# Kernel optimization log

Hardware: AMD Instinct MI355X
Metric: run time of the kernel (lower is better)

The kernel has to match this reference:

```python
import jax, jax.numpy as jnp
import numpy as np

N_NODES = 50000
N_EDGES = 800000
D = 128          # node_dim == hidden_dim (heads=1, concat -> hidden_dim)
N_LAYERS = 3
NUM_GRAPHS = 512


def setup_inputs() -> dict:
    key = jax.random.key(0)
    ks = jax.random.split(key, 12)
    x = jax.random.normal(ks[0], (N_NODES, D), dtype=jnp.float32)
    edge_index = jax.random.randint(ks[1], (2, N_EDGES), 0, N_NODES, dtype=jnp.int64)
    batch = jnp.sort(jax.random.randint(ks[2], (N_NODES,), 0, NUM_GRAPHS, dtype=jnp.int64))
    s = 1.0 / np.sqrt(D)
    # stacked per-layer params (all layers are D->D since node_dim==hidden_dim)
    Wq = jax.random.normal(ks[3], (N_LAYERS, D, D), dtype=jnp.float32) * s
    Wk = jax.random.normal(ks[4], (N_LAYERS, D, D), dtype=jnp.float32) * s
    Wv = jax.random.normal(ks[5], (N_LAYERS, D, D), dtype=jnp.float32) * s
    Ws = jax.random.normal(ks[6], (N_LAYERS, D, D), dtype=jnp.float32) * s  # lin_skip (root weight)
    bq = jnp.zeros((N_LAYERS, D), dtype=jnp.float32)
    bk = jnp.zeros((N_LAYERS, D), dtype=jnp.float32)
    bv = jnp.zeros((N_LAYERS, D), dtype=jnp.float32)
    bs = jnp.zeros((N_LAYERS, D), dtype=jnp.float32)
    return dict(x=x, edge_index=edge_index, batch=batch,
                Wq=Wq, bq=bq, Wk=Wk, bk=bk, Wv=Wv, bv=bv, Ws=Ws, bs=bs)


def _transformer_conv(x, src, dst, Wq, bq, Wk, bk, Wv, bv, Ws, bs):
    # PyG TransformerConv, heads=1, concat=True, root_weight=True, no edge_attr
    q = x @ Wq.T + bq                     # [N, D]
    k = x @ Wk.T + bk                     # [N, D]
    v = x @ Wv.T + bv                     # [N, D]
    scale = 1.0 / jnp.sqrt(jnp.asarray(D, x.dtype))
    alpha = jnp.sum(q[dst] * k[src], axis=-1) * scale           # [E]
    # scatter-softmax over edges sharing the same destination node
    amax = jax.ops.segment_max(alpha, dst, num_segments=N_NODES)  # [N]
    ex = jnp.exp(alpha - amax[dst])                               # [E]
    denom = jax.ops.segment_sum(ex, dst, num_segments=N_NODES)    # [N]
    w = ex / denom[dst]                                           # [E]
    out = jax.ops.segment_sum(w[:, None] * v[src], dst, num_segments=N_NODES)  # [N, D]
    return out + (x @ Ws.T + bs)          # skip connection (lin_skip)


def reference(x, edge_index, batch, Wq, bq, Wk, bk, Wv, bv, Ws, bs):
    src, dst = edge_index[0], edge_index[1]
    for l in range(N_LAYERS):
        x = jax.nn.relu(_transformer_conv(x, src, dst,
                                          Wq[l], bq[l], Wk[l], bk[l],
                                          Wv[l], bv[l], Ws[l], bs[l]))
    # global_mean_pool
    sums = jax.ops.segment_sum(x, batch, num_segments=NUM_GRAPHS)          # [G, D]
    counts = jax.ops.segment_sum(jnp.ones((x.shape[0],), x.dtype), batch,
                                 num_segments=NUM_GRAPHS)                  # [G]
    return sums / jnp.maximum(counts, 1.0)[:, None]
```

## Files before the change

kernel.cpp:

```cpp
#include <hip/hip_runtime.h>
#include <hip/hip_fp8.h>

#define N_NODES 50000
#define N_EDGES 800000
#define DIM 128
#define NLAYERS 3
#define NGRAPH 512
#define SCAN_NB ((N_NODES + 255) / 256)
#define NBUCK   ((N_NODES + 255) / 256)
#define P1_CHUNK 2048
#define P1_EPT   8
#define P1_NB    ((N_EDGES + P1_CHUNK - 1) / P1_CHUNK)

typedef __attribute__((ext_vector_type(8)))  __bf16 bf16x8;
typedef __attribute__((ext_vector_type(16))) float  f32x16;
typedef __attribute__((ext_vector_type(2)))  float  f32x2;

union U8 { uint2 u; unsigned char b[8]; };

__device__ inline void cvt8_pk(U8 x, f32x2* f) {
#if defined(__has_builtin) && __has_builtin(__builtin_amdgcn_cvt_pk_f32_fp8)
    f[0] = __builtin_amdgcn_cvt_pk_f32_fp8(x.u.x, false);
    f[1] = __builtin_amdgcn_cvt_pk_f32_fp8(x.u.x, true);
    f[2] = __builtin_amdgcn_cvt_pk_f32_fp8(x.u.y, false);
    f[3] = __builtin_amdgcn_cvt_pk_f32_fp8(x.u.y, true);
#else
#pragma unroll
    for (int j = 0; j < 4; ++j) {
        __hip_fp8_e4m3 a; a.__x = x.b[2 * j];
        __hip_fp8_e4m3 c; c.__x = x.b[2 * j + 1];
        f32x2 r; r[0] = (float)a; r[1] = (float)c;
        f[j] = r;
    }
#endif
}

__device__ inline uint4 pack16_fp8(const float* v) {
    uint4 r;
    unsigned int* pr = (unsigned int*)&r;
#if defined(__has_builtin) && __has_builtin(__builtin_amdgcn_cvt_pk_fp8_f32)
#pragma unroll
    for (int w = 0; w < 4; ++w) {
        int o = 0;
        o = __builtin_amdgcn_cvt_pk_fp8_f32(v[4 * w + 0], v[4 * w + 1], o, false);
        o = __builtin_amdgcn_cvt_pk_fp8_f32(v[4 * w + 2], v[4 * w + 3], o, true);
        pr[w] = (unsigned int)o;
    }
#else
#pragma unroll
    for (int w = 0; w < 4; ++w) {
        unsigned int o = 0;
#pragma unroll
        for (int j = 0; j < 4; ++j) {
            __hip_fp8_e4m3 t8(v[4 * w + j]);
            o |= ((unsigned int)t8.__x) << (8 * j);
        }
        pr[w] = o;
    }
#endif
    return r;
}

__global__ __launch_bounds__(256) void k_cast(const float* __restrict__ in,
                                              __bf16* __restrict__ out, int n) {
    int i = blockIdx.x * blockDim.x + threadIdx.x;
    int base = i * 8;
    if (base >= n) return;
    float4 a = *(const float4*)(in + base);
    float4 b = *(const float4*)(in + base + 4);
    bf16x8 o;
    o[0] = (__bf16)a.x; o[1] = (__bf16)a.y; o[2] = (__bf16)a.z; o[3] = (__bf16)a.w;
    o[4] = (__bf16)b.x; o[5] = (__bf16)b.y; o[6] = (__bf16)b.z; o[7] = (__bf16)b.w;
    *(bf16x8*)(out + base) = o;
}

__global__ __launch_bounds__(256) void k_castW(
    const float* __restrict__ i0, const float* __restrict__ i1,
    const float* __restrict__ i2, const float* __restrict__ i3,
    __bf16* __restrict__ o0, __bf16* __restrict__ o1,
    __bf16* __restrict__ o2, __bf16* __restrict__ o3) {
    int sel = blockIdx.y;
    const float* in = (sel == 0) ? i0 : (sel == 1) ? i1 : (sel == 2) ? i2 : i3;
    __bf16* out     = (sel == 0) ? o0 : (sel == 1) ? o1 : (sel == 2) ? o2 : o3;
    int i = blockIdx.x * 256 + threadIdx.x;
    if (i >= NLAYERS * 2048) return;
    int layer = i >> 11;
    int w = i & 2047;
    int ct = w >> 9, kt = (w >> 6) & 7, lane = w & 63;
    int row = ct * 32 + (lane & 31);
    int col = kt * 16 + (lane >> 5) * 8;
    const float* srcp = in + (size_t)layer * DIM * DIM + row * DIM + col;
    float4 a = *(const float4*)srcp;
    float4 b = *(const float4*)(srcp + 4);
    bf16x8 o;
    o[0] = (__bf16)a.x; o[1] = (__bf16)a.y; o[2] = (__bf16)a.z; o[3] = (__bf16)a.w;
    o[4] = (__bf16)b.x; o[5] = (__bf16)b.y; o[6] = (__bf16)b.z; o[7] = (__bf16)b.w;
    *(bf16x8*)(out + (size_t)i * 8) = o;
}

__global__ __launch_bounds__(256) void k_degree(const int* __restrict__ dst,
                                                int* __restrict__ cnt) {
    int i = blockIdx.x * blockDim.x + threadIdx.x;
    if (i < N_EDGES) atomicAdd(&cnt[dst[i]], 1);
}

__global__ __launch_bounds__(256) void k_scan1(const int* __restrict__ cnt,
                                               int* __restrict__ off,
                                               int* __restrict__ bsum) {
    __shared__ int s[256];
    int b = blockIdx.x, t = threadIdx.x;
    int i = b * 256 + t;
    int v = (i < N_NODES) ? cnt[i] : 0;
    s[t] = v; __syncthreads();
#pragma unroll
    for (int d = 1; d < 256; d <<= 1) {
        int nv = (t >= d) ? s[t - d] : 0;
        __syncthreads();
        s[t] += nv;
        __syncthreads();
    }
    if (i < N_NODES) off[i] = s[t] - v;
    if (t == 255) bsum[b] = s[255];
}

__global__ __launch_bounds__(256) void k_scan2(const int* __restrict__ bsum,
                                               int* __restrict__ boff,
                                               int* __restrict__ offN) {
    __shared__ int s[256];
    int t = threadIdx.x;
    int v = (t < SCAN_NB) ? bsum[t] : 0;
    s[t] = v; __syncthreads();
#pragma unroll
    for (int d = 1; d < 256; d <<= 1) {
        int nv = (t >= d) ? s[t - d] : 0;
        __syncthreads();
        s[t] += nv;
        __syncthreads();
    }
    boff[t] = s[t] - v;
    if (t == 255) *offN = s[255];
}

__global__ __launch_bounds__(256) void k_scan3(int* __restrict__ off,
                                               const int* __restrict__ boff) {
    int b = blockIdx.x, t = threadIdx.x;
    int i = b * 256 + t;
    if (i < N_NODES) off[i] += boff[b];
}

__global__ __launch_bounds__(256) void k_ginit(const int* __restrict__ off,
                                               int* __restrict__ gcursor) {
    int t = threadIdx.x;
    if (t < NBUCK) gcursor[t] = off[t * 256];
}

__global__ __launch_bounds__(256) void k_bucket(const int* __restrict__ src,
                                                const int* __restrict__ dst,
                                                int* __restrict__ gcursor,
                                                unsigned long long* __restrict__ pairs) {
    __shared__ int lcount[256];
    __shared__ int lstart[256];
    __shared__ int lresv[256];
    __shared__ unsigned long long stage[P1_CHUNK];
    int t = threadIdx.x;
    int base = blockIdx.x * P1_CHUNK;
    int cnt = N_EDGES - base; if (cnt > P1_CHUNK) cnt = P1_CHUNK;

    lcount[t] = 0;
    __syncthreads();

    int my_s[P1_EPT], my_d[P1_EPT], my_b[P1_EPT];
#pragma unroll
    for (int j = 0; j < P1_EPT; ++j) {
        int idx = t + j * 256;
        if (idx < cnt) {
            my_s[j] = src[base + idx];
            my_d[j] = dst[base + idx];
            my_b[j] = my_d[j] >> 8;
            atomicAdd(&lcount[my_b[j]], 1);
        } else my_b[j] = -1;
    }
    __syncthreads();

    int v = lcount[t];
    lstart[t] = v;
    __syncthreads();
#pragma unroll
    for (int d = 1; d < 256; d <<= 1) {
        int nv = (t >= d) ? lstart[t - d] : 0;
        __syncthreads();
        lstart[t] += nv;
        __syncthreads();
    }
    int excl = lstart[t] - v;
    __syncthreads();
    lstart[t] = excl;
    lresv[t] = (t < NBUCK && v > 0) ? atomicAdd(&gcursor[t], v) : 0;
    lcount[t] = 0;
    __syncthreads();

#pragma unroll
    for (int j = 0; j < P1_EPT; ++j) {
        if (my_b[j] >= 0) {
            int lpos = lstart[my_b[j]] + atomicAdd(&lcount[my_b[j]], 1);
            stage[lpos] = ((unsigned long long)(unsigned)my_d[j] << 32) | (unsigned)my_s[j];
        }
    }
    __syncthreads();

    for (int sl = t; sl < cnt; sl += 256) {
        unsigned long long pr = stage[sl];
        int d_ = (int)(pr >> 32);
        int b_ = d_ >> 8;
        int g = lresv[b_] + (sl - lstart[b_]);
        pairs[g] = pr;
    }
}

__global__ __launch_bounds__(256) void k_csr(const unsigned long long* __restrict__ pairs,
                                             const int* __restrict__ off,
                                             int* __restrict__ src_s) {
    __shared__ int cur[256];
    int b = blockIdx.x, t = threadIdx.x;
    int nb0 = b * 256;
    int nb1 = nb0 + 256; if (nb1 > N_NODES) nb1 = N_NODES;
    int e0 = off[nb0], e1 = off[nb1];
    cur[t] = 0;
    __syncthreads();
    for (int e = e0 + t; e < e1; e += 256) {
        unsigned long long pr = pairs[e];
        int d_ = (int)(pr >> 32);
        int s_ = (int)(pr & 0xffffffffu);
        int pos = off[d_] + atomicAdd(&cur[d_ & 255], 1);
        src_s[pos] = s_;
    }
}

__global__ __launch_bounds__(256) void k_gemm_fused(
    const __bf16* __restrict__ Xb,
    const __bf16* __restrict__ Wq, const __bf16* __restrict__ Wk,
    const __bf16* __restrict__ Wv, const __bf16* __restrict__ Wsk,
    const float* __restrict__ Bq, const float* __restrict__ Bk,
    const float* __restrict__ Bv, const float* __restrict__ Bs,
    __bf16* __restrict__ Oq, unsigned char* __restrict__ Okv,
    __bf16* __restrict__ Osk) {
    __shared__ uint4 At[32][16];
    __shared__ float lt[4][32][33];
    int t = threadIdx.x;
    int wsel = t >> 6, l = t & 63;
    int lo5 = l & 31, hi = l >> 5;
    int row0 = blockIdx.x * 32;

    const __bf16* W = (wsel == 0) ? Wq : (wsel == 1) ? Wk : (wsel == 2) ? Wv : Wsk;
    const float*  B = (wsel == 0) ? Bq : (wsel == 1) ? Bk : (wsel == 2) ? Bv : Bs;

    {
        int r = t >> 3;
        int u0 = (t & 7) * 2;
        int grow = row0 + r;
        uint4 a0 = {}, a1 = {};
        if (grow < N_NODES) {
            const uint4* gp = (const uint4*)(Xb + (size_t)grow * DIM);
            a0 = gp[u0]; a1 = gp[u0 + 1];
        }
        At[r][u0 ^ (r & 15)]       = a0;
        At[r][(u0 + 1) ^ (r & 15)] = a1;
    }
    __syncthreads();

    bf16x8 a[8];
#pragma unroll
    for (int kt = 0; kt < 8; ++kt)
        a[kt] = *(const bf16x8*)&At[lo5][(kt * 2 + hi) ^ (lo5 & 15)];

    int rr = l >> 1, h = l & 1;
    int grow = row0 + rr;
    bool rok = (grow < N_NODES);

#pragma unroll
    for (int ct = 0; ct < 4; ++ct) {
        int col0 = ct * 32;
        const bf16x8* bp = (const bf16x8*)W + (size_t)(ct * 8) * 64 + l;
        f32x16 acc0 = {}, acc1 = {};
#pragma unroll
        for (int kt = 0; kt < 4; ++kt) {
            acc0 = __builtin_amdgcn_mfma_f32_32x32x16_bf16(a[kt],     bp[(size_t)kt * 64],       acc0, 0, 0, 0);
            acc1 = __builtin_amdgcn_mfma_f32_32x32x16_bf16(a[kt + 4], bp[(size_t)(kt + 4) * 64], acc1, 0, 0, 0);
        }
        f32x16 acc = acc0 + acc1;

        float bias = B[col0 + lo5];
#pragma unroll
        for (int r = 0; r < 16; ++r) {
            int rl = (r & 3) + 8 * (r >> 2) + 4 * hi;
            lt[wsel][rl][lo5] = acc[r] + bias;
        }
        __syncthreads();

        float vals[16];
#pragma unroll
        for (int j = 0; j < 16; ++j) vals[j] = lt[wsel][rr][h * 16 + j];

        if (rok) {
            int gcol = col0 + h * 16;
            if (wsel == 0 || wsel == 3) {
                __bf16* O = (wsel == 0) ? Oq : Osk;
                bf16x8 o0, o1;
#pragma unroll
                for (int j = 0; j < 8; ++j) { o0[j] = (__bf16)vals[j]; o1[j] = (__bf16)vals[8 + j]; }
                bf16x8* orow = (bf16x8*)(O + (size_t)grow * DIM + gcol);
                orow[0] = o0; orow[1] = o1;
            } else {
                int coff = (wsel == 2) ? 128 : 0;
                uint4 pk = pack16_fp8(vals);
                *(uint4*)(Okv + (size_t)grow * 256 + coff + gcol) = pk;
            }
        }
        __syncthreads();
    }
}

__global__ __launch_bounds__(256) void k_edge_fused(const __bf16* __restrict__ q,
                                                    const unsigned char* __restrict__ kv,
                                                    const __bf16* __restrict__ skip,
                                                    const int* __restrict__ src_s,
                                                    const int* __restrict__ off,
                                                    float* __restrict__ xout,
                                                    __bf16* __restrict__ xb,
                                                    int wf32) {
    int t = threadIdx.x;
    int wave = t >> 6, l = t & 63;
    int n = blockIdx.x * 4 + wave;
    if (n >= N_NODES) return;
    int g = l >> 4, gl = l & 15;
    int start = off[n], end = off[n + 1];

    const float S = 0.08838834764831845f;
    f32x2 qf[4];
    {
        bf16x8 qv = *(const bf16x8*)(q + (size_t)n * DIM + gl * 8);
#pragma unroll
        for (int j = 0; j < 4; ++j) {
            f32x2 r;
            r[0] = (float)qv[2 * j] * S;
            r[1] = (float)qv[2 * j + 1] * S;
            qf[j] = r;
        }
    }

    float denom = 0.f;
    f32x2 facc[4] = {};

    for (int e = start + g; e < end; e += 8) {
        int s0 = src_s[e];
        bool h1 = (e + 4 < end);
        int s1 = h1 ? src_s[e + 4] : s0;
        const unsigned char* r0 = kv + (size_t)s0 * 256 + gl * 8;
        const unsigned char* r1 = kv + (size_t)s1 * 256 + gl * 8;
        U8 k0u, k1u, v0u, v1u;
        k0u.u = *(const uint2*)(r0);
        k1u.u = *(const uint2*)(r1);
        v0u.u = *(const uint2*)(r0 + 128);
        v1u.u = *(const uint2*)(r1 + 128);

        f32x2 k0f[4], k1f[4];
        cvt8_pk(k0u, k0f);
        cvt8_pk(k1u, k1f);
        f32x2 d0 = qf[0] * k0f[0];
        f32x2 d1 = qf[0] * k1f[0];
        d0 += qf[1] * k0f[1];  d1 += qf[1] * k1f[1];
        d0 += qf[2] * k0f[2];  d1 += qf[2] * k1f[2];
        d0 += qf[3] * k0f[3];  d1 += qf[3] * k1f[3];
        float p0 = d0[0] + d0[1];
        float p1 = d1[0] + d1[1];
        p0 += __shfl_xor(p0, 8, 16);  p1 += __shfl_xor(p1, 8, 16);
        p0 += __shfl_xor(p0, 4, 16);  p1 += __shfl_xor(p1, 4, 16);
        p0 += __shfl_xor(p0, 2, 16);  p1 += __shfl_xor(p1, 2, 16);
        p0 += __shfl_xor(p0, 1, 16);  p1 += __shfl_xor(p1, 1, 16);
        p0 = fminf(p0, 80.f);
        p1 = h1 ? fminf(p1, 80.f) : -INFINITY;

        float w0 = __expf(p0);
        float w1 = __expf(p1);
        denom += w0 + w1;

        f32x2 v0f[4], v1f[4];
        cvt8_pk(v0u, v0f);
        cvt8_pk(v1u, v1f);
        f32x2 w02; w02[0] = w0; w02[1] = w0;
        f32x2 w12; w12[0] = w1; w12[1] = w1;
#pragma unroll
        for (int j = 0; j < 4; ++j)
            facc[j] += w02 * v0f[j] + w12 * v1f[j];
    }

#pragma unroll
    for (int dlt = 16; dlt <= 32; dlt <<= 1) {
        denom += __shfl_xor(denom, dlt, 64);
#pragma unroll
        for (int j = 0; j < 4; ++j) {
            f32x2 o;
            o[0] = __shfl_xor(facc[j][0], dlt, 64);
            o[1] = __shfl_xor(facc[j][1], dlt, 64);
            facc[j] += o;
        }
    }
    float inv = (denom > 0.f) ? 1.f / denom : 0.f;

    if (g == 0) {
        bf16x8 sk = *(const bf16x8*)(skip + (size_t)n * DIM + gl * 8);
        float o[8];
        bf16x8 ob;
#pragma unroll
        for (int j = 0; j < 8; ++j) {
            float f = facc[j >> 1][j & 1];
            float val = fmaxf((float)sk[j] + f * inv, 0.f);
            o[j] = val; ob[j] = (__bf16)val;
        }
        if (wf32) {
            float* xrow = xout + (size_t)n * DIM + gl * 8;
            *(float4*)(xrow)     = make_float4(o[0], o[1], o[2], o[3]);
            *(float4*)(xrow + 4) = make_float4(o[4], o[5], o[6], o[7]);
        }
        *(bf16x8*)(xb + (size_t)n * DIM + gl * 8) = ob;
    }
}

__global__ __launch_bounds__(256) void k_pool(const float* __restrict__ x,
                                              const int* __restrict__ batch,
                                              float* __restrict__ out) {
    __shared__ float sacc[4][DIM];
    int g = blockIdx.x;
    int t = threadIdx.x;
    int w = t >> 6, l = t & 63;
    int lo = 0, hi = N_NODES;
    while (lo < hi) { int mid = (lo + hi) >> 1; if (batch[mid] < g) lo = mid + 1; else hi = mid; }
    int s0 = lo;
    hi = N_NODES;
    while (lo < hi) { int mid = (lo + hi) >> 1; if (batch[mid] < g + 1) lo = mid + 1; else hi = mid; }
    int s1 = lo;
    float a0 = 0.f, a1 = 0.f;
    for (int n = s0 + w; n < s1; n += 4) {
        float2 xr = *(const float2*)(x + (size_t)n * DIM + l * 2);
        a0 += xr.x; a1 += xr.y;
    }
    sacc[w][l * 2] = a0; sacc[w][l * 2 + 1] = a1;
    __syncthreads();
    if (t < DIM) {
        float s = sacc[0][t] + sacc[1][t] + sacc[2][t] + sacc[3][t];
        int cnt = s1 - s0;
        out[(size_t)g * DIM + t] = s / (float)((cnt > 0) ? cnt : 1);
    }
}

extern "C" void kernel_launch(void* const* d_in, const int* in_sizes, int n_in,
                              void* d_out, int out_size, void* d_ws, size_t ws_size,
                              hipStream_t stream) {
    const float* x0   = (const float*)d_in[0];
    const int*  eidx  = (const int*)d_in[1];
    const int*  batch = (const int*)d_in[2];
    const float* Wq = (const float*)d_in[3];
    const float* bq = (const float*)d_in[4];
    const float* Wk = (const float*)d_in[5];
    const float* bk = (const float*)d_in[6];
    const float* Wv = (const float*)d_in[7];
    const float* bv = (const float*)d_in[8];
    const float* Ws = (const float*)d_in[9];
    const float* bs = (const float*)d_in[10];
    float* out = (float*)d_out;

    const int* src = eidx;
    const int* dst = eidx + N_EDGES;

    char* ws = (char*)d_ws;
    size_t p = 0;
    auto alloc = [&](size_t bytes) -> void* {
        void* r = ws + p;
        p = (p + bytes + 255) & ~(size_t)255;
        return r;
    };
    int*    off    = (int*)alloc((N_NODES + 1) * sizeof(int));
    int*    cnt    = (int*)alloc(N_NODES * sizeof(int));
    int*    bsum   = (int*)alloc(256 * sizeof(int));
    int*    boff   = (int*)alloc(256 * sizeof(int));
    int*    gcur   = (int*)alloc(256 * sizeof(int));
    int*    src_s  = (int*)alloc(N_EDGES * sizeof(int));
    unsigned long long* prs = (unsigned long long*)alloc((size_t)N_EDGES * 8);
    __bf16* Xb     = (__bf16*)alloc((size_t)N_NODES * DIM * sizeof(__bf16));
    __bf16* qb     = (__bf16*)alloc((size_t)N_NODES * DIM * sizeof(__bf16));
    unsigned char* kvb = (unsigned char*)alloc((size_t)N_NODES * 256);
    __bf16* skb    = (__bf16*)alloc((size_t)N_NODES * DIM * sizeof(__bf16));
    float*  s1     = (float*)alloc((size_t)N_NODES * DIM * sizeof(float));
    __bf16* Wqb    = (__bf16*)alloc((size_t)NLAYERS * DIM * DIM * sizeof(__bf16));
    __bf16* Wkb    = (__bf16*)alloc((size_t)NLAYERS * DIM * DIM * sizeof(__bf16));
    __bf16* Wvb    = (__bf16*)alloc((size_t)NLAYERS * DIM * DIM * sizeof(__bf16));
    __bf16* Wsb    = (__bf16*)alloc((size_t)NLAYERS * DIM * DIM * sizeof(__bf16));

    {
        int nx = N_NODES * DIM;
        k_cast<<<(nx / 8 + 255) / 256, 256, 0, stream>>>(x0, Xb, nx);
        dim3 gw((NLAYERS * 2048 + 255) / 256, 4);
        k_castW<<<gw, 256, 0, stream>>>(Wq, Wk, Wv, Ws, Wqb, Wkb, Wvb, Wsb);
    }

    hipMemsetAsync(cnt, 0, N_NODES * sizeof(int), stream);
    k_degree<<<(N_EDGES + 255) / 256, 256, 0, stream>>>(dst, cnt);
    k_scan1<<<SCAN_NB, 256, 0, stream>>>(cnt, off, bsum);
    k_scan2<<<1, 256, 0, stream>>>(bsum, boff, off + N_NODES);
    k_scan3<<<SCAN_NB, 256, 0, stream>>>(off, boff);
    k_ginit<<<1, 256, 0, stream>>>(off, gcur);
    k_bucket<<<P1_NB, 256, 0, stream>>>(src, dst, gcur, prs);
    k_csr<<<NBUCK, 256, 0, stream>>>(prs, off, src_s);

    for (int l = 0; l < NLAYERS; ++l) {
        const __bf16* wq = Wqb + (size_t)l * DIM * DIM;
        const __bf16* wk = Wkb + (size_t)l * DIM * DIM;
        const __bf16* wv = Wvb + (size_t)l * DIM * DIM;
        const __bf16* wsk = Wsb + (size_t)l * DIM * DIM;
        const float* biq = bq + (size_t)l * DIM;
        const float* bik = bk + (size_t)l * DIM;
        const float* biv = bv + (size_t)l * DIM;
        const float* bis = bs + (size_t)l * DIM;

        k_gemm_fused<<<(N_NODES + 31) / 32, 256, 0, stream>>>(Xb, wq, wk, wv, wsk,
                                                              biq, bik, biv, bis,
                                                              qb, kvb, skb);
        int wf32 = (l == NLAYERS - 1) ? 1 : 0;
        k_edge_fused<<<(N_NODES + 3) / 4, 256, 0, stream>>>(qb, kvb, skb, src_s, off,
                                                            s1, Xb, wf32);
    }

    k_pool<<<NGRAPH, 256, 0, stream>>>(s1, batch, out);
}
```

Baseline: 278.2 us.

## Interleave K/V fp8 rows and unroll edge gather to four edges per iteration

The projection kernel now writes K and V fp8 values interleaved in 16-byte units (8 K bytes then 8 V bytes per 8 columns), so the edge kernel fetches each lane's K and V slices with one 16-byte load instead of two separate 8-byte loads. The edge loop also processes four edges per group per iteration instead of two, giving more independent gathers in flight to hide memory latency. The costs are higher register pressure and more masked work on the tail for nodes with low degree.

```diff
diff --git a/kernel.cpp b/kernel.cpp
--- a/kernel.cpp
+++ b/kernel.cpp
@@ -35,12 +35,12 @@
 #endif
 }
 
-__device__ inline uint4 pack16_fp8(const float* v) {
-    uint4 r;
+__device__ inline uint2 pack8_fp8(const float* v) {
+    uint2 r;
     unsigned int* pr = (unsigned int*)&r;
 #if defined(__has_builtin) && __has_builtin(__builtin_amdgcn_cvt_pk_fp8_f32)
 #pragma unroll
-    for (int w = 0; w < 4; ++w) {
+    for (int w = 0; w < 2; ++w) {
         int o = 0;
         o = __builtin_amdgcn_cvt_pk_fp8_f32(v[4 * w + 0], v[4 * w + 1], o, false);
         o = __builtin_amdgcn_cvt_pk_fp8_f32(v[4 * w + 2], v[4 * w + 3], o, true);
@@ -48,7 +48,7 @@
     }
 #else
 #pragma unroll
-    for (int w = 0; w < 4; ++w) {
+    for (int w = 0; w < 2; ++w) {
         unsigned int o = 0;
 #pragma unroll
         for (int j = 0; j < 4; ++j) {
@@ -311,9 +311,13 @@
                 bf16x8* orow = (bf16x8*)(O + (size_t)grow * DIM + gcol);
                 orow[0] = o0; orow[1] = o1;
             } else {
-                int coff = (wsel == 2) ? 128 : 0;
-                uint4 pk = pack16_fp8(vals);
-                *(uint4*)(Okv + (size_t)grow * 256 + coff + gcol) = pk;
+                int koff = (wsel == 2) ? 8 : 0;
+                int unit = gcol >> 3;
+                uint2 lo8 = pack8_fp8(vals);
+                uint2 hi8 = pack8_fp8(vals + 8);
+                unsigned char* base = Okv + (size_t)grow * 256;
+                *(uint2*)(base + unit * 16 + koff)        = lo8;
+                *(uint2*)(base + (unit + 1) * 16 + koff)  = hi8;
             }
         }
         __syncthreads();
@@ -351,47 +355,76 @@
     float denom = 0.f;
     f32x2 facc[4] = {};
 
-    for (int e = start + g; e < end; e += 8) {
+    for (int e = start + g; e < end; e += 16) {
         int s0 = src_s[e];
-        bool h1 = (e + 4 < end);
-        int s1 = h1 ? src_s[e + 4] : s0;
-        const unsigned char* r0 = kv + (size_t)s0 * 256 + gl * 8;
-        const unsigned char* r1 = kv + (size_t)s1 * 256 + gl * 8;
-        U8 k0u, k1u, v0u, v1u;
-        k0u.u = *(const uint2*)(r0);
-        k1u.u = *(const uint2*)(r1);
-        v0u.u = *(const uint2*)(r0 + 128);
-        v1u.u = *(const uint2*)(r1 + 128);
-
-        f32x2 k0f[4], k1f[4];
-        cvt8_pk(k0u, k0f);
-        cvt8_pk(k1u, k1f);
-        f32x2 d0 = qf[0] * k0f[0];
-        f32x2 d1 = qf[0] * k1f[0];
-        d0 += qf[1] * k0f[1];  d1 += qf[1] * k1f[1];
-        d0 += qf[2] * k0f[2];  d1 += qf[2] * k1f[2];
-        d0 += qf[3] * k0f[3];  d1 += qf[3] * k1f[3];
-        float p0 = d0[0] + d0[1];
-        float p1 = d1[0] + d1[1];
-        p0 += __shfl_xor(p0, 8, 16);  p1 += __shfl_xor(p1, 8, 16);
-        p0 += __shfl_xor(p0, 4, 16);  p1 += __shfl_xor(p1, 4, 16);
-        p0 += __shfl_xor(p0, 2, 16);  p1 += __shfl_xor(p1, 2, 16);
-        p0 += __shfl_xor(p0, 1, 16);  p1 += __shfl_xor(p1, 1, 16);
+        bool h1 = (e + 4 < end), h2 = (e + 8 < end), h3 = (e + 12 < end);
+        int s1 = h1 ? src_s[e + 4]  : s0;
+        int s2 = h2 ? src_s[e + 8]  : s0;
+        int s3 = h3 ? src_s[e + 12] : s0;
+        uint4 r0 = *(const uint4*)(kv + (size_t)s0 * 256 + gl * 16);
+        uint4 r1 = *(const uint4*)(kv + (size_t)s1 * 256 + gl * 16);
+        uint4 r2 = *(const uint4*)(kv + (size_t)s2 * 256 + gl * 16);
+        uint4 r3 = *(const uint4*)(kv + (size_t)s3 * 256 + gl * 16);
+
+        U8 ku; f32x2 kf[4];
+        float p0, p1, p2, p3;
+        {
+            ku.u = make_uint2(r0.x, r0.y); cvt8_pk(ku, kf);
+            f32x2 d = qf[0]*kf[0] + qf[1]*kf[1] + qf[2]*kf[2] + qf[3]*kf[3];
+            p0 = d[0] + d[1];
+        }
+        {
+            ku.u = make_uint2(r1.x, r1.y); cvt8_pk(ku, kf);
+            f32x2 d = qf[0]*kf[0] + qf[1]*kf[1] + qf[2]*kf[2] + qf[3]*kf[3];
+            p1 = d[0] + d[1];
+        }
+        {
+            ku.u = make_uint2(r2.x, r2.y); cvt8_pk(ku, kf);
+            f32x2 d = qf[0]*kf[0] + qf[1]*kf[1] + qf[2]*kf[2] + qf[3]*kf[3];
+            p2 = d[0] + d[1];
+        }
+        {
+            ku.u = make_uint2(r3.x, r3.y); cvt8_pk(ku, kf);
+            f32x2 d = qf[0]*kf[0] + qf[1]*kf[1] + qf[2]*kf[2] + qf[3]*kf[3];
+            p3 = d[0] + d[1];
+        }
+        p0 += __shfl_xor(p0, 8, 16); p1 += __shfl_xor(p1, 8, 16);
+        p2 += __shfl_xor(p2, 8, 16); p3 += __shfl_xor(p3, 8, 16);
+        p0 += __shfl_xor(p0, 4, 16); p1 += __shfl_xor(p1, 4, 16);
+        p2 += __shfl_xor(p2, 4, 16); p3 += __shfl_xor(p3, 4, 16);
+        p0 += __shfl_xor(p0, 2, 16); p1 += __shfl_xor(p1, 2, 16);
+        p2 += __shfl_xor(p2, 2, 16); p3 += __shfl_xor(p3, 2, 16);
+        p0 += __shfl_xor(p0, 1, 16); p1 += __shfl_xor(p1, 1, 16);
+        p2 += __shfl_xor(p2, 1, 16); p3 += __shfl_xor(p3, 1, 16);
         p0 = fminf(p0, 80.f);
         p1 = h1 ? fminf(p1, 80.f) : -INFINITY;
+        p2 = h2 ? fminf(p2, 80.f) : -INFINITY;
+        p3 = h3 ? fminf(p3, 80.f) : -INFINITY;
 
         float w0 = __expf(p0);
         float w1 = __expf(p1);
-        denom += w0 + w1;
-
-        f32x2 v0f[4], v1f[4];
-        cvt8_pk(v0u, v0f);
-        cvt8_pk(v1u, v1f);
-        f32x2 w02; w02[0] = w0; w02[1] = w0;
-        f32x2 w12; w12[0] = w1; w12[1] = w1;
-#pragma unroll
-        for (int j = 0; j < 4; ++j)
-            facc[j] += w02 * v0f[j] + w12 * v1f[j];
+        float w2 = __expf(p2);
+        float w3 = __expf(p3);
+        denom += (w0 + w1) + (w2 + w3);
+
+        U8 vu; f32x2 vf[4];
+        f32x2 ww;
+        ww[0] = w0; ww[1] = w0;
+        vu.u = make_uint2(r0.z, r0.w); cvt8_pk(vu, vf);
+#pragma unroll
+        for (int j = 0; j < 4; ++j) facc[j] += ww * vf[j];
+        ww[0] = w1; ww[1] = w1;
+        vu.u = make_uint2(r1.z, r1.w); cvt8_pk(vu, vf);
+#pragma unroll
+        for (int j = 0; j < 4; ++j) facc[j] += ww * vf[j];
+        ww[0] = w2; ww[1] = w2;
+        vu.u = make_uint2(r2.z, r2.w); cvt8_pk(vu, vf);
+#pragma unroll
+        for (int j = 0; j < 4; ++j) facc[j] += ww * vf[j];
+        ww[0] = w3; ww[1] = w3;
+        vu.u = make_uint2(r3.z, r3.w); cvt8_pk(vu, vf);
+#pragma unroll
+        for (int j = 0; j < 4; ++j) facc[j] += ww * vf[j];
     }
 
 #pragma unroll
```

Result: slower. 284.6 us (+2.3%).
